# Performance work log

Measured on AMD Instinct MI355X. Metric: run time of the kernel, lower is better.

## Reference

```python
import jax, jax.numpy as jnp
import numpy as np

B, T, M, E, H, D = 4, 1024, 1024, 1024, 16, 64
SCALE = D ** (-0.5)


def setup_inputs() -> dict:
    key = jax.random.key(0)
    ks = jax.random.split(key, 8)
    w = 0.02  # weight scale for numerical stability of softmax
    return {
        "x": jax.random.normal(ks[0], (B, T, E), jnp.float32),
        "xl_memory": jax.random.normal(ks[1], (B, M, 2, H * D), jnp.float32),
        "relative_positions": jax.random.normal(ks[2], (H, T, M + T), jnp.float32),
        "Wq": jax.random.normal(ks[3], (E, H * D), jnp.float32) * w,
        "bq": jnp.zeros((H * D,), jnp.float32),
        "Wk": jax.random.normal(ks[4], (E, H * D), jnp.float32) * w,
        "bk": jnp.zeros((H * D,), jnp.float32),
        "Wv": jax.random.normal(ks[5], (E, H * D), jnp.float32) * w,
        "bv": jnp.zeros((H * D,), jnp.float32),
        "Wo": jax.random.normal(ks[6], (H * D, E), jnp.float32) * w,
        "bo": jnp.zeros((E,), jnp.float32),
    }


def reference(x, xl_memory, relative_positions, Wq, bq, Wk, bk, Wv, bv, Wo, bo):
    b, t, _ = x.shape
    q = (x @ Wq + bq) * SCALE                     # [b, t, H*D] (scale applied to queries)
    k = x @ Wk + bk
    v = x @ Wv + bv
    k_xl = xl_memory[:, :, 0]                      # [b, m, H*D]
    v_xl = xl_memory[:, :, 1]
    m = k_xl.shape[1]
    keys = jnp.concatenate((k_xl, k), axis=1)      # [b, j, H*D], j = m + t
    values = jnp.concatenate((v_xl, v), axis=1)
    j = keys.shape[1]

    qh = q.reshape(b, t, H, D).transpose(0, 2, 1, 3)       # b h i d
    kh = keys.reshape(b, j, H, D).transpose(0, 2, 1, 3)    # b h j d
    vh = values.reshape(b, j, H, D).transpose(0, 2, 1, 3)  # b h j d

    qk = jnp.einsum("bhid,bhjd->bhij", qh, kh)
    qk = relative_positions[..., -t:, -j:] + qk
    qk = qk * SCALE                                # second scale, faithful to source
    mask = jnp.triu(jnp.ones((t, j), dtype=bool), j - t + 1)
    qk = jnp.where(mask, -jnp.inf, qk)
    attn = jax.nn.softmax(qk, axis=-1)             # dropout p=0.0 -> identity

    qkv = jnp.einsum("bhij,bhjd->bhid", attn, vh)
    qkv = qkv.transpose(0, 2, 1, 3).reshape(b, t, H * D)
    out = qkv @ Wo + bo

    kv_memories = jnp.stack((keys, values), axis=-2)  # [b, j, 2, H*D]
    kv_to_add_xl = kv_memories[:, -m:]                 # [b, m, 2, H*D]
    return out, kv_to_add_xl
```

## Files before the change

### kernel.cpp

```cpp
#include <hip/hip_runtime.h>
#include <hip/hip_bf16.h>

typedef unsigned short u16;
typedef unsigned int u32;
typedef __attribute__((ext_vector_type(8))) short short8;
typedef __attribute__((ext_vector_type(4))) float f32x4;

#define B_ 4
#define T_ 1024
#define E_ 1024
#define NH 16
#define HD 1024
#define JTOT 2048
#define SCALE 0.125f
#define LOG2E 1.44269504f

__device__ __forceinline__ u16 f2b(float f) {
  u32 x = __float_as_uint(f);
  u32 r = (x + 0x7fffu + ((x >> 16) & 1u)) >> 16;
  return (u16)r;
}
__device__ __forceinline__ u16 f2b_fast(float f) {
  return (u16)((__float_as_uint(f) + 0x8000u) >> 16);
}
__device__ __forceinline__ float fexp2(float x) {
  float r;
  asm("v_exp_f32 %0, %1" : "=v"(r) : "v"(x));
  return r;
}

__device__ __forceinline__ void gload_lds16(const void* g, void* l) {
  __builtin_amdgcn_global_load_lds((const __attribute__((address_space(1))) u32*)g,
                                   (__attribute__((address_space(3))) u32*)l, 16, 0, 0);
}

__device__ __forceinline__ short8 pack8(float4 f0, float4 f1) {
  short8 o;
  o[0] = (short)f2b(f0.x); o[1] = (short)f2b(f0.y);
  o[2] = (short)f2b(f0.z); o[3] = (short)f2b(f0.w);
  o[4] = (short)f2b(f1.x); o[5] = (short)f2b(f1.y);
  o[6] = (short)f2b(f1.z); o[7] = (short)f2b(f1.w);
  return o;
}

__global__ __launch_bounds__(256) void cvt_bf16(const float* __restrict__ in,
                                                u16* __restrict__ out, int n8) {
  int i = blockIdx.x * 256 + threadIdx.x;
  if (i >= n8) return;
  const float4* p = (const float4*)in + (size_t)i * 2;
  ((short8*)out)[i] = pack8(p[0], p[1]);
}

__global__ __launch_bounds__(256) void cvt_w4T(const float* __restrict__ Wq, const float* __restrict__ Wk,
                                               const float* __restrict__ Wv, const float* __restrict__ Wo,
                                               u16* __restrict__ wqkvT, u16* __restrict__ woT) {
  __shared__ float tile[64][65];
  const float* W;
  u16* WT;
  int z = blockIdx.z;
  if (z == 0) { W = Wq; WT = wqkvT; }
  else if (z == 1) { W = Wk; WT = wqkvT + (size_t)1024 * 1024; }
  else if (z == 2) { W = Wv; WT = wqkvT + (size_t)2048 * 1024; }
  else { W = Wo; WT = woT; }
  int t = threadIdx.x;
  int r0 = blockIdx.y * 64, c0 = blockIdx.x * 64;
#pragma unroll
  for (int i = 0; i < 16; ++i) {
    int r = i * 4 + (t >> 6), c = t & 63;
    tile[r][c] = W[(size_t)(r0 + r) * 1024 + c0 + c];
  }
  __syncthreads();
#pragma unroll
  for (int i = 0; i < 16; ++i) {
    int r = i * 4 + (t >> 6), c = t & 63;
    WT[(size_t)(c0 + r) * 1024 + r0 + c] = f2b(tile[c][r]);
  }
}

__global__ __launch_bounds__(256) void cvt_xl_k(const float* __restrict__ xl, u16* __restrict__ kt) {
  int i = blockIdx.x * 256 + threadIdx.x;
  int hd8 = i & 127, j = (i >> 7) & 1023, b = i >> 17;
  const float4* p = (const float4*)(xl + ((((size_t)b * 1024 + j) * 2 + 0) * 1024 + (size_t)hd8 * 8));
  short8 o = pack8(p[0], p[1]);
  int h = hd8 >> 3, d0 = (hd8 & 7) * 8;
  int jc = j >> 6, jl = j & 63;
  u16* dst = kt + (((size_t)(b * 16 + h) * 32 + jc) * 4096) + jl * 64 + (d0 ^ (((jl >> 2) & 3) << 4));
  *(short8*)dst = o;
}

__global__ __launch_bounds__(256) void cvt_xl_vT(const float* __restrict__ xl, u16* __restrict__ vt) {
  __shared__ u16 Vl[64 * 72];
  int bx = blockIdx.x;
  int jc = bx & 15, h = (bx >> 4) & 15, b = bx >> 8;
  int t = threadIdx.x;
  int j0 = jc * 64;
#pragma unroll
  for (int it = 0; it < 2; ++it) {
    int p = t + 256 * it;
    int j = p >> 3, d8 = p & 7;
    const float4* src = (const float4*)(xl + ((((size_t)b * 1024 + j0 + j) * 2 + 1) * 1024 + h * 64 + (size_t)d8 * 8));
    *(short8*)&Vl[j * 72 + d8 * 8] = pack8(src[0], src[1]);
  }
  __syncthreads();
#pragma unroll
  for (int it = 0; it < 2; ++it) {
    int p = t + 256 * it;
    int d = p >> 3, j8 = p & 7;
    short8 o;
#pragma unroll
    for (int e = 0; e < 8; ++e) o[e] = (short)Vl[(j8 * 8 + e) * 72 + d];
    u16* dst = vt + (((size_t)(b * 16 + h) * 32 + jc) * 4096) + d * 64 + ((j8 * 8) ^ (((d >> 2) & 3) << 4));
    *(short8*)dst = o;
  }
}

__global__ __launch_bounds__(256) void trans_vnew(const u16* __restrict__ vb, u16* __restrict__ vt) {
  __shared__ u16 Vl[64 * 72];
  int bx = blockIdx.x;
  int jcl = bx & 15, h = (bx >> 4) & 15, b = bx >> 8;
  int jc = 16 + jcl;
  int t = threadIdx.x;
  int t0 = jcl * 64;
#pragma unroll
  for (int it = 0; it < 2; ++it) {
    int p = t + 256 * it;
    int j = p >> 3, d8 = p & 7;
    *(short8*)&Vl[j * 72 + d8 * 8] =
        *(const short8*)&vb[((size_t)b * 1024 + t0 + j) * 1024 + h * 64 + d8 * 8];
  }
  __syncthreads();
#pragma unroll
  for (int it = 0; it < 2; ++it) {
    int p = t + 256 * it;
    int d = p >> 3, j8 = p & 7;
    short8 o;
#pragma unroll
    for (int e = 0; e < 8; ++e) o[e] = (short)Vl[(j8 * 8 + e) * 72 + d];
    u16* dst = vt + (((size_t)(b * 16 + h) * 32 + jc) * 4096) + d * 64 + ((j8 * 8) ^ (((d >> 2) & 3) << 4));
    *(short8*)dst = o;
  }
}

template <int MODE>
__global__ __launch_bounds__(256) void gemm128(
    const u16* __restrict__ A, const u16* __restrict__ BT,
    const float* __restrict__ b0, const float* __restrict__ b1, const float* __restrict__ b2,
    u16* __restrict__ qb, float* __restrict__ kvout, u16* __restrict__ kt, u16* __restrict__ vb,
    float* __restrict__ outf, int Ntiles, int Kdim) {
  __shared__ __align__(16) u16 As[128 * 32];
  __shared__ __align__(16) u16 Bs[128 * 32];
  const int t = threadIdx.x;
  const int lane = t & 63, wv = t >> 6;
  const int wr = wv >> 1, wc = wv & 1;
  const int m0 = (blockIdx.x / Ntiles) * 128;
  const int n0 = (blockIdx.x % Ntiles) * 128;
  const int lr = lane & 15, lg = lane >> 4;

  f32x4 acc[4][4] = {};

  for (int kc = 0; kc < Kdim; kc += 32) {
    __syncthreads();
#pragma unroll
    for (int i = 0; i < 2; ++i) {
      int p = t + 256 * i;
      gload_lds16(A + (size_t)(m0 + (p >> 2)) * Kdim + kc + (p & 3) * 8, &As[p * 8]);
    }
#pragma unroll
    for (int i = 0; i < 2; ++i) {
      int p = t + 256 * i;
      gload_lds16(BT + (size_t)(n0 + (p >> 2)) * Kdim + kc + (p & 3) * 8, &Bs[p * 8]);
    }
    __syncthreads();

    short8 af[4], bf[4];
#pragma unroll
    for (int mf = 0; mf < 4; ++mf)
      af[mf] = *(const short8*)&As[(wr * 64 + mf * 16 + lr) * 32 + lg * 8];
#pragma unroll
    for (int nf = 0; nf < 4; ++nf)
      bf[nf] = *(const short8*)&Bs[(wc * 64 + nf * 16 + lr) * 32 + lg * 8];
#pragma unroll
    for (int mf = 0; mf < 4; ++mf)
#pragma unroll
      for (int nf = 0; nf < 4; ++nf)
        acc[mf][nf] = __builtin_amdgcn_mfma_f32_16x16x32_bf16(af[mf], bf[nf], acc[mf][nf], 0, 0, 0);
  }

#pragma unroll
  for (int mf = 0; mf < 4; ++mf) {
#pragma unroll
    for (int nf = 0; nf < 4; ++nf) {
#pragma unroll
      for (int r = 0; r < 4; ++r) {
        int row = m0 + wr * 64 + mf * 16 + lg * 4 + r;
        int col = n0 + wc * 64 + nf * 16 + lr;
        float v = acc[mf][nf][r];
        if (MODE == 0) {
          int b = row >> 10, tt = row & 1023;
          if (col < 1024) {
            v += b0[col];
            qb[(size_t)row * HD + col] = f2b(v * (SCALE * SCALE * LOG2E));
          } else if (col < 2048) {
            int hd = col - 1024;
            v += b1[hd];
            kvout[((size_t)(b * 1024 + tt) * 2 + 0) * HD + hd] = v;
            int h = hd >> 6, d = hd & 63, jl = tt & 63, jc = 16 + (tt >> 6);
            kt[(((size_t)(b * 16 + h) * 32 + jc) * 4096) + jl * 64 + (d ^ (((jl >> 2) & 3) << 4))] = f2b(v);
          } else {
            int hd = col - 2048;
            v += b2[hd];
            kvout[((size_t)(b * 1024 + tt) * 2 + 1) * HD + hd] = v;
            vb[((size_t)b * 1024 + tt) * 1024 + hd] = f2b(v);
          }
        } else {
          outf[(size_t)row * E_ + col] = v + b0[col];
        }
      }
    }
  }
}

__global__ __launch_bounds__(256) void attn_kernel(
    const u16* __restrict__ qb, const u16* __restrict__ kt, const u16* __restrict__ vt,
    const float* __restrict__ rel, u16* __restrict__ aout) {
  __shared__ __align__(16) u16 Ks[2][4096];
  __shared__ __align__(16) u16 Vs[2][4096];
  __shared__ __align__(16) u16 Pl[4096];
  const int bx = blockIdx.x;
  const int b = bx & 3, h = (bx >> 2) & 15, qt = bx >> 6;
  const int i0 = qt * 64;
  const int t = threadIdx.x, lane = t & 63, w = t >> 6;
  const int lr = lane & 15, lg = lane >> 4;
  const int sel = (lr >> 2) & 3;
  const float RC = SCALE * LOG2E;

  const u16* ktb = kt + (size_t)(b * 16 + h) * 32 * 4096;
  const u16* vtb = vt + (size_t)(b * 16 + h) * 32 * 4096;
  const float* relbase = rel + (size_t)h * T_ * JTOT;
  const int ib = i0 + w * 16 + lg * 4;

  short8 qf[2];
#pragma unroll
  for (int kc = 0; kc < 2; ++kc)
    qf[kc] = *(const short8*)&qb[(size_t)(b * T_ + i0 + w * 16 + lr) * HD + h * 64 + kc * 32 + lg * 8];

  short8 vf5;
#pragma unroll
  for (int e = 0; e < 8; ++e) vf5[e] = (lr == 0) ? (short)0x3f80 : (short)0;

  const int nchunks = qt + 17;

  auto stage = [&](int buf, int jc2) {
    const u16* ksrc = ktb + (size_t)jc2 * 4096;
    const u16* vsrc = vtb + (size_t)jc2 * 4096;
    gload_lds16(ksrc + t * 8, &Ks[buf][t * 8]);
    gload_lds16(ksrc + (t + 256) * 8, &Ks[buf][(t + 256) * 8]);
    gload_lds16(vsrc + t * 8, &Vs[buf][t * 8]);
    gload_lds16(vsrc + (t + 256) * 8, &Vs[buf][(t + 256) * 8]);
  };

  float rl[4][4];
  auto loadrel = [&](int j0) {
#pragma unroll
    for (int nf = 0; nf < 4; ++nf)
#pragma unroll
      for (int r = 0; r < 4; ++r)
        rl[nf][r] = relbase[(size_t)(ib + r) * JTOT + j0 + nf * 16 + lr];
  };

  stage(0, 0);
  loadrel(0);

  f32x4 o[5] = {};
  float mrow[4];
#pragma unroll
  for (int r = 0; r < 4; ++r) mrow[r] = -__builtin_inff();

  int cur = 0;
  for (int jc = 0; jc < nchunks; ++jc) {
    __syncthreads();
    if (jc + 1 < nchunks) stage(cur ^ 1, jc + 1);

    f32x4 s4[4] = {};
#pragma unroll
    for (int nf = 0; nf < 4; ++nf)
#pragma unroll
      for (int kc = 0; kc < 2; ++kc) {
        short8 kf = *(const short8*)&Ks[cur][(nf * 16 + lr) * 64 + ((kc * 32 + lg * 8) ^ (sel << 4))];
        s4[nf] = __builtin_amdgcn_mfma_f32_16x16x32_bf16(qf[kc], kf, s4[nf], 0, 0, 0);
      }

    float p[4][4], lmax[4];
    const bool domask = (jc == qt + 16);
#pragma unroll
    for (int nf = 0; nf < 4; ++nf)
#pragma unroll
      for (int r = 0; r < 4; ++r) {
        float v = fmaf(rl[nf][r], RC, s4[nf][r]);
        if (domask && (nf * 16 + lr) > (w * 16 + lg * 4 + r)) v = -__builtin_inff();
        p[nf][r] = v;
      }
#pragma unroll
    for (int r = 0; r < 4; ++r)
      lmax[r] = fmaxf(fmaxf(p[0][r], p[1][r]), fmaxf(p[2][r], p[3][r]));
    if (jc + 1 < nchunks) loadrel((jc + 1) * 64);

    float need = -__builtin_inff();
#pragma unroll
    for (int r = 0; r < 4; ++r) need = fmaxf(need, lmax[r] - mrow[r]);
    const bool dores = !__all(need <= 11.0f);
    if (dores) {
      float chmax[4], sc[4];
#pragma unroll
      for (int r = 0; r < 4; ++r) chmax[r] = lmax[r];
#pragma unroll
      for (int msk = 1; msk <= 8; msk <<= 1)
#pragma unroll
        for (int r = 0; r < 4; ++r)
          chmax[r] = fmaxf(chmax[r], __shfl_xor(chmax[r], msk, 64));
#pragma unroll
      for (int r = 0; r < 4; ++r) {
        float nm = fmaxf(mrow[r], chmax[r]);
        sc[r] = fexp2(mrow[r] - nm);
        mrow[r] = nm;
      }
#pragma unroll
      for (int nf = 0; nf < 5; ++nf)
#pragma unroll
        for (int r = 0; r < 4; ++r) o[nf][r] *= sc[r];
    }

#pragma unroll
    for (int nf = 0; nf < 4; ++nf)
#pragma unroll
      for (int r = 0; r < 4; ++r) {
        float pe = fexp2(p[nf][r] - mrow[r]);
        Pl[(w * 16 + lg * 4 + r) * 64 + (((nf ^ lg) << 4) + lr)] = f2b_fast(pe);
      }

#pragma unroll
    for (int kc = 0; kc < 2; ++kc) {
      const int pcol = (kc * 32 + lg * 8) ^ (sel << 4);
      short8 pa = *(const short8*)&Pl[(w * 16 + lr) * 64 + pcol];
#pragma unroll
      for (int nf = 0; nf < 4; ++nf) {
        short8 vf = *(const short8*)&Vs[cur][(nf * 16 + lr) * 64 + pcol];
        o[nf] = __builtin_amdgcn_mfma_f32_16x16x32_bf16(pa, vf, o[nf], 0, 0, 0);
      }
      o[4] = __builtin_amdgcn_mfma_f32_16x16x32_bf16(pa, vf5, o[4], 0, 0, 0);
    }
    cur ^= 1;
  }

  float inv[4];
#pragma unroll
  for (int r = 0; r < 4; ++r)
    inv[r] = 1.0f / __shfl(o[4][r], lane & 48, 64);
#pragma unroll
  for (int nf = 0; nf < 4; ++nf)
#pragma unroll
    for (int r = 0; r < 4; ++r) {
      int i = i0 + w * 16 + lg * 4 + r, d = nf * 16 + lr;
      aout[(size_t)(b * T_ + i) * HD + h * 64 + d] = f2b_fast(o[nf][r] * inv[r]);
    }
}

extern "C" void kernel_launch(void* const* d_in, const int* in_sizes, int n_in,
                              void* d_out, int out_size, void* d_ws, size_t ws_size,
                              hipStream_t stream) {
  const float* x  = (const float*)d_in[0];
  const float* xl = (const float*)d_in[1];
  const float* rel = (const float*)d_in[2];
  const float* Wq = (const float*)d_in[3];
  const float* bq = (const float*)d_in[4];
  const float* Wk = (const float*)d_in[5];
  const float* bk = (const float*)d_in[6];
  const float* Wv = (const float*)d_in[7];
  const float* bv = (const float*)d_in[8];
  const float* Wo = (const float*)d_in[9];
  const float* bo = (const float*)d_in[10];

  float* out = (float*)d_out;
  float* kvout = out + (size_t)B_ * T_ * E_;

  char* ws = (char*)d_ws;
  u16* xb    = (u16*)ws; ws += (size_t)4096 * 1024 * 2;
  u16* wqkvT = (u16*)ws; ws += (size_t)3072 * 1024 * 2;
  u16* woT   = (u16*)ws; ws += (size_t)1024 * 1024 * 2;
  u16* qbuf  = (u16*)ws; ws += (size_t)4096 * 1024 * 2;
  u16* kt    = (u16*)ws; ws += (size_t)B_ * NH * 32 * 4096 * 2;
  u16* vt    = (u16*)ws; ws += (size_t)B_ * NH * 32 * 4096 * 2;
  u16* vbn   = (u16*)ws; ws += (size_t)4096 * 1024 * 2;
  u16* aout  = (u16*)ws; ws += (size_t)4096 * 1024 * 2;

  cvt_bf16<<<2048, 256, 0, stream>>>(x, xb, 524288);
  cvt_w4T<<<dim3(16, 16, 4), 256, 0, stream>>>(Wq, Wk, Wv, Wo, wqkvT, woT);
  cvt_xl_k<<<2048, 256, 0, stream>>>(xl, kt);
  cvt_xl_vT<<<1024, 256, 0, stream>>>(xl, vt);

  gemm128<0><<<32 * 24, 256, 0, stream>>>(xb, wqkvT, bq, bk, bv,
                                          qbuf, kvout, kt, vbn, nullptr, 24, 1024);
  trans_vnew<<<1024, 256, 0, stream>>>(vbn, vt);
  attn_kernel<<<1024, 256, 0, stream>>>(qbuf, kt, vt, rel, aout);
  gemm128<1><<<32 * 8, 256, 0, stream>>>(aout, woT, bo, nullptr, nullptr,
                                         nullptr, nullptr, nullptr, nullptr, out, 8, 1024);
}
```

Before: 218.6 us.

## Split GEMM variants, add coalesced kv expand, tune attention barrier and priority

Splits the templated GEMM into a QKV kernel and an output-projection kernel. The QKV kernel now writes bf16 K/V to a staging buffer, and a separate kv_expand kernel writes the fp32 kv memory output with wide coalesced stores instead of scattered fp32 stores. The output GEMM uses 64-row tiles so 512 blocks launch and more CUs are busy. The attention loop replaces __syncthreads with a partial vmcnt wait plus a raw s_barrier and raises wave priority around the MFMA sections, so the next chunk's loads can stay in flight. The cost is an extra launch and extra memory traffic for the bf16 round trip, and K/V memory outputs are now rounded to bf16 before being widened back to fp32.

Measured after the change: 219.6 us. No clear change (+0.5%).

```diff
diff --git a/kernel.cpp b/kernel.cpp
--- a/kernel.cpp
+++ b/kernel.cpp
@@ -22,6 +22,9 @@
 }
 __device__ __forceinline__ u16 f2b_fast(float f) {
   return (u16)((__float_as_uint(f) + 0x8000u) >> 16);
+}
+__device__ __forceinline__ float b2f(u16 b) {
+  return __uint_as_float((u32)b << 16);
 }
 __device__ __forceinline__ float fexp2(float x) {
   float r;
@@ -141,34 +144,32 @@
   }
 }
 
-template <int MODE>
-__global__ __launch_bounds__(256) void gemm128(
+__global__ __launch_bounds__(256) void gemm_qkv(
     const u16* __restrict__ A, const u16* __restrict__ BT,
     const float* __restrict__ b0, const float* __restrict__ b1, const float* __restrict__ b2,
-    u16* __restrict__ qb, float* __restrict__ kvout, u16* __restrict__ kt, u16* __restrict__ vb,
-    float* __restrict__ outf, int Ntiles, int Kdim) {
+    u16* __restrict__ qb, u16* __restrict__ kbp, u16* __restrict__ kt, u16* __restrict__ vb) {
   __shared__ __align__(16) u16 As[128 * 32];
   __shared__ __align__(16) u16 Bs[128 * 32];
   const int t = threadIdx.x;
   const int lane = t & 63, wv = t >> 6;
   const int wr = wv >> 1, wc = wv & 1;
-  const int m0 = (blockIdx.x / Ntiles) * 128;
-  const int n0 = (blockIdx.x % Ntiles) * 128;
+  const int m0 = (blockIdx.x / 24) * 128;
+  const int n0 = (blockIdx.x % 24) * 128;
   const int lr = lane & 15, lg = lane >> 4;
 
   f32x4 acc[4][4] = {};
 
-  for (int kc = 0; kc < Kdim; kc += 32) {
+  for (int kc = 0; kc < 1024; kc += 32) {
     __syncthreads();
 #pragma unroll
     for (int i = 0; i < 2; ++i) {
       int p = t + 256 * i;
-      gload_lds16(A + (size_t)(m0 + (p >> 2)) * Kdim + kc + (p & 3) * 8, &As[p * 8]);
+      gload_lds16(A + (size_t)(m0 + (p >> 2)) * 1024 + kc + (p & 3) * 8, &As[p * 8]);
     }
 #pragma unroll
     for (int i = 0; i < 2; ++i) {
       int p = t + 256 * i;
-      gload_lds16(BT + (size_t)(n0 + (p >> 2)) * Kdim + kc + (p & 3) * 8, &Bs[p * 8]);
+      gload_lds16(BT + (size_t)(n0 + (p >> 2)) * 1024 + kc + (p & 3) * 8, &Bs[p * 8]);
     }
     __syncthreads();
 
@@ -195,29 +196,92 @@
         int row = m0 + wr * 64 + mf * 16 + lg * 4 + r;
         int col = n0 + wc * 64 + nf * 16 + lr;
         float v = acc[mf][nf][r];
-        if (MODE == 0) {
-          int b = row >> 10, tt = row & 1023;
-          if (col < 1024) {
-            v += b0[col];
-            qb[(size_t)row * HD + col] = f2b(v * (SCALE * SCALE * LOG2E));
-          } else if (col < 2048) {
-            int hd = col - 1024;
-            v += b1[hd];
-            kvout[((size_t)(b * 1024 + tt) * 2 + 0) * HD + hd] = v;
-            int h = hd >> 6, d = hd & 63, jl = tt & 63, jc = 16 + (tt >> 6);
-            kt[(((size_t)(b * 16 + h) * 32 + jc) * 4096) + jl * 64 + (d ^ (((jl >> 2) & 3) << 4))] = f2b(v);
-          } else {
-            int hd = col - 2048;
-            v += b2[hd];
-            kvout[((size_t)(b * 1024 + tt) * 2 + 1) * HD + hd] = v;
-            vb[((size_t)b * 1024 + tt) * 1024 + hd] = f2b(v);
-          }
+        int b = row >> 10, tt = row & 1023;
+        if (col < 1024) {
+          v += b0[col];
+          qb[(size_t)row * HD + col] = f2b(v * (SCALE * SCALE * LOG2E));
+        } else if (col < 2048) {
+          int hd = col - 1024;
+          u16 kv16 = f2b(v + b1[hd]);
+          kbp[(size_t)(b * 1024 + tt) * 1024 + hd] = kv16;
+          int h = hd >> 6, d = hd & 63, jl = tt & 63, jc = 16 + (tt >> 6);
+          kt[(((size_t)(b * 16 + h) * 32 + jc) * 4096) + jl * 64 + (d ^ (((jl >> 2) & 3) << 4))] = kv16;
         } else {
-          outf[(size_t)row * E_ + col] = v + b0[col];
+          int hd = col - 2048;
+          vb[(size_t)(b * 1024 + tt) * 1024 + hd] = f2b(v + b2[hd]);
         }
       }
     }
   }
+}
+
+__global__ __launch_bounds__(256) void kv_expand(const u16* __restrict__ kbp, const u16* __restrict__ vbp,
+                                                 float* __restrict__ kvout) {
+  int i = blockIdx.x * 256 + threadIdx.x;
+  int hd8 = i & 127, tt = (i >> 7) & 1023, b = i >> 17;
+  size_t src = ((size_t)(b * 1024 + tt)) * 1024 + (size_t)hd8 * 8;
+  short8 k8 = *(const short8*)&kbp[src];
+  short8 v8 = *(const short8*)&vbp[src];
+  float4 k0, k1, v0, v1;
+#pragma unroll
+  for (int e = 0; e < 4; ++e) {
+    ((float*)&k0)[e] = b2f((u16)k8[e]); ((float*)&k1)[e] = b2f((u16)k8[e + 4]);
+    ((float*)&v0)[e] = b2f((u16)v8[e]); ((float*)&v1)[e] = b2f((u16)v8[e + 4]);
+  }
+  float* kdst = kvout + (((size_t)(b * 1024 + tt) * 2 + 0) * 1024) + hd8 * 8;
+  float* vdst = kvout + (((size_t)(b * 1024 + tt) * 2 + 1) * 1024) + hd8 * 8;
+  ((float4*)kdst)[0] = k0; ((float4*)kdst)[1] = k1;
+  ((float4*)vdst)[0] = v0; ((float4*)vdst)[1] = v1;
+}
+
+__global__ __launch_bounds__(256) void gemm_out(
+    const u16* __restrict__ A, const u16* __restrict__ BT,
+    const float* __restrict__ bias, float* __restrict__ outf) {
+  __shared__ __align__(16) u16 As[64 * 32];
+  __shared__ __align__(16) u16 Bs[128 * 32];
+  const int t = threadIdx.x;
+  const int lane = t & 63, wv = t >> 6;
+  const int wr = wv >> 1, wc = wv & 1;
+  const int m0 = (blockIdx.x >> 3) * 64;
+  const int n0 = (blockIdx.x & 7) * 128;
+  const int lr = lane & 15, lg = lane >> 4;
+
+  f32x4 acc[2][4] = {};
+
+  for (int kc = 0; kc < 1024; kc += 32) {
+    __syncthreads();
+    gload_lds16(A + (size_t)(m0 + (t >> 2)) * 1024 + kc + (t & 3) * 8, &As[t * 8]);
+#pragma unroll
+    for (int i = 0; i < 2; ++i) {
+      int p = t + 256 * i;
+      gload_lds16(BT + (size_t)(n0 + (p >> 2)) * 1024 + kc + (p & 3) * 8, &Bs[p * 8]);
+    }
+    __syncthreads();
+
+    short8 af[2], bf[4];
+#pragma unroll
+    for (int mf = 0; mf < 2; ++mf)
+      af[mf] = *(const short8*)&As[(wr * 32 + mf * 16 + lr) * 32 + lg * 8];
+#pragma unroll
+    for (int nf = 0; nf < 4; ++nf)
+      bf[nf] = *(const short8*)&Bs[(wc * 64 + nf * 16 + lr) * 32 + lg * 8];
+#pragma unroll
+    for (int mf = 0; mf < 2; ++mf)
+#pragma unroll
+      for (int nf = 0; nf < 4; ++nf)
+        acc[mf][nf] = __builtin_amdgcn_mfma_f32_16x16x32_bf16(af[mf], bf[nf], acc[mf][nf], 0, 0, 0);
+  }
+
+#pragma unroll
+  for (int mf = 0; mf < 2; ++mf)
+#pragma unroll
+    for (int nf = 0; nf < 4; ++nf)
+#pragma unroll
+      for (int r = 0; r < 4; ++r) {
+        int row = m0 + wr * 32 + mf * 16 + lg * 4 + r;
+        int col = n0 + wc * 64 + nf * 16 + lr;
+        outf[(size_t)row * E_ + col] = acc[mf][nf][r] + bias[col];
+      }
 }
 
 __global__ __launch_bounds__(256) void attn_kernel(
@@ -248,7 +312,7 @@
 #pragma unroll
   for (int e = 0; e < 8; ++e) vf5[e] = (lr == 0) ? (short)0x3f80 : (short)0;
 
-  const int nchunks = qt + 17;
+  const int nch = qt + 17;
 
   auto stage = [&](int buf, int jc2) {
     const u16* ksrc = ktb + (size_t)jc2 * 4096;
@@ -269,6 +333,7 @@
   };
 
   stage(0, 0);
+  asm volatile("" ::: "memory");
   loadrel(0);
 
   f32x4 o[5] = {};
@@ -277,11 +342,15 @@
   for (int r = 0; r < 4; ++r) mrow[r] = -__builtin_inff();
 
   int cur = 0;
-  for (int jc = 0; jc < nchunks; ++jc) {
-    __syncthreads();
-    if (jc + 1 < nchunks) stage(cur ^ 1, jc + 1);
+  for (int jc = 0; jc < nch; ++jc) {
+    asm volatile("s_waitcnt vmcnt(16)" ::: "memory");
+    __builtin_amdgcn_sched_barrier(0);
+    asm volatile("s_barrier" ::: "memory");
+    if (jc + 1 < nch) stage(cur ^ 1, jc + 1);
+    asm volatile("" ::: "memory");
 
     f32x4 s4[4] = {};
+    __builtin_amdgcn_s_setprio(1);
 #pragma unroll
     for (int nf = 0; nf < 4; ++nf)
 #pragma unroll
@@ -289,6 +358,7 @@
         short8 kf = *(const short8*)&Ks[cur][(nf * 16 + lr) * 64 + ((kc * 32 + lg * 8) ^ (sel << 4))];
         s4[nf] = __builtin_amdgcn_mfma_f32_16x16x32_bf16(qf[kc], kf, s4[nf], 0, 0, 0);
       }
+    __builtin_amdgcn_s_setprio(0);
 
     float p[4][4], lmax[4];
     const bool domask = (jc == qt + 16);
@@ -303,7 +373,7 @@
 #pragma unroll
     for (int r = 0; r < 4; ++r)
       lmax[r] = fmaxf(fmaxf(p[0][r], p[1][r]), fmaxf(p[2][r], p[3][r]));
-    if (jc + 1 < nchunks) loadrel((jc + 1) * 64);
+    if (jc + 1 < nch) loadrel((jc + 1) * 64);
 
     float need = -__builtin_inff();
 #pragma unroll
@@ -338,6 +408,7 @@
         Pl[(w * 16 + lg * 4 + r) * 64 + (((nf ^ lg) << 4) + lr)] = f2b_fast(pe);
       }
 
+    __builtin_amdgcn_s_setprio(1);
 #pragma unroll
     for (int kc = 0; kc < 2; ++kc) {
       const int pcol = (kc * 32 + lg * 8) ^ (sel << 4);
@@ -349,6 +420,8 @@
       }
       o[4] = __builtin_amdgcn_mfma_f32_16x16x32_bf16(pa, vf5, o[4], 0, 0, 0);
     }
+    __builtin_amdgcn_s_setprio(0);
+    asm volatile("" ::: "memory");
     cur ^= 1;
   }
 
@@ -391,6 +464,7 @@
   u16* kt    = (u16*)ws; ws += (size_t)B_ * NH * 32 * 4096 * 2;
   u16* vt    = (u16*)ws; ws += (size_t)B_ * NH * 32 * 4096 * 2;
   u16* vbn   = (u16*)ws; ws += (size_t)4096 * 1024 * 2;
+  u16* kbp   = (u16*)ws; ws += (size_t)4096 * 1024 * 2;
   u16* aout  = (u16*)ws; ws += (size_t)4096 * 1024 * 2;
 
   cvt_bf16<<<2048, 256, 0, stream>>>(x, xb, 524288);
@@ -398,10 +472,9 @@
   cvt_xl_k<<<2048, 256, 0, stream>>>(xl, kt);
   cvt_xl_vT<<<1024, 256, 0, stream>>>(xl, vt);
 
-  gemm128<0><<<32 * 24, 256, 0, stream>>>(xb, wqkvT, bq, bk, bv,
-                                          qbuf, kvout, kt, vbn, nullptr, 24, 1024);
+  gemm_qkv<<<32 * 24, 256, 0, stream>>>(xb, wqkvT, bq, bk, bv, qbuf, kbp, kt, vbn);
+  kv_expand<<<2048, 256, 0, stream>>>(kbp, vbn, kvout);
   trans_vnew<<<1024, 256, 0, stream>>>(vbn, vt);
   attn_kernel<<<1024, 256, 0, stream>>>(qbuf, kt, vt, rel, aout);
-  gemm128<1><<<32 * 8, 256, 0, stream>>>(aout, woT, bo, nullptr, nullptr,
-                                         nullptr, nullptr, nullptr, nullptr, out, 8, 1024);
-}
+  gemm_out<<<512, 256, 0, stream>>>(aout, woT, bo, out);
+}
```
